# Kernel tuning notes

Measured on AMD Instinct MI355X. Metric: run time of the kernel, lower is better.

The kernel has to match this reference:

```python
import jax, jax.numpy as jnp
import numpy as np

B, T, D, H = 2, 2048, 1024, 16
Hd = D // H


def setup_inputs() -> dict:
    key = jax.random.key(0)
    ks = jax.random.split(key, 9)
    s = 1.0 / np.sqrt(D)
    return {
        "x": jax.random.normal(ks[0], (B, T, D), jnp.float32),
        "Wq": jax.random.normal(ks[1], (D, D), jnp.float32) * s,
        "bq": jax.random.normal(ks[2], (D,), jnp.float32) * 0.01,
        "Wk": jax.random.normal(ks[3], (D, D), jnp.float32) * s,
        "bk": jax.random.normal(ks[4], (D,), jnp.float32) * 0.01,
        "Wv": jax.random.normal(ks[5], (D, D), jnp.float32) * s,
        "bv": jax.random.normal(ks[6], (D,), jnp.float32) * 0.01,
        "Wo": jax.random.normal(ks[7], (D, D), jnp.float32) * s,
        "bo": jax.random.normal(ks[8], (D,), jnp.float32) * 0.01,
    }


def reference(x, Wq, bq, Wk, bk, Wv, bv, Wo, bo):
    # torch Linear: y = x @ W.T + b
    def proj(W, b):
        y = jnp.einsum('btd,ed->bte', x, W) + b          # [B,T,D]
        return y.reshape(B, T, H, Hd).transpose(0, 2, 1, 3)  # [B,H,T,Hd]
    q = proj(Wq, bq) / jnp.sqrt(jnp.asarray(Hd, x.dtype))
    k = proj(Wk, bk)
    v = proj(Wv, bv)
    scores = jnp.einsum('bhqd,bhkd->bhqk', q, k)         # [B,H,T,T]
    attn = jax.nn.softmax(scores, axis=-1)
    out = jnp.einsum('bhqk,bhkd->bhqd', attn, v)         # [B,H,T,Hd]
    out = out.transpose(0, 2, 1, 3).reshape(B, T, D)
    return jnp.einsum('btd,ed->bte', out, Wo) + bo
```

## Files before the change

kernel.cpp:

```cpp
#include <hip/hip_runtime.h>
#include <cmath>

typedef __attribute__((ext_vector_type(8))) short bf16x8;
typedef __attribute__((ext_vector_type(4))) float f32x4;

#define MFMA_BF16 __builtin_amdgcn_mfma_f32_16x16x32_bf16

__device__ __forceinline__ unsigned short f2b(float f) {
  union { float f; unsigned u; } v; v.f = f;
  unsigned r = (v.u + 0x7FFFu + ((v.u >> 16) & 1u)) >> 16;
  return (unsigned short)r;
}

__device__ __forceinline__ unsigned cvt_pk_bf16(float lo, float hi) {
  unsigned r;
  asm("v_cvt_pk_bf16_f32 %0, %1, %2" : "=v"(r) : "v"(lo), "v"(hi));
  return r;
}

__device__ __forceinline__ float fast_exp2(float x) {
  float r;
  asm("v_exp_f32 %0, %1" : "=v"(r) : "v"(x));
  return r;
}

__device__ __forceinline__ void gload_lds16(const void* g, void* l) {
  __builtin_amdgcn_global_load_lds(
      (const __attribute__((address_space(1))) void*)g,
      (__attribute__((address_space(3))) void*)l, 16, 0, 0);
}

__global__ __launch_bounds__(256) void cvt_all(
    const float* __restrict__ x, const float* __restrict__ Wq,
    const float* __restrict__ Wk, const float* __restrict__ Wv,
    const float* __restrict__ Wo,
    unsigned short* __restrict__ xb, unsigned short* __restrict__ wqb,
    unsigned short* __restrict__ wkb, unsigned short* __restrict__ wvb,
    unsigned short* __restrict__ wob) {
  int i = blockIdx.x * 256 + threadIdx.x;
  const float* src; unsigned short* dst; int off;
  if (i < 1048576)      { src = x;  dst = xb;  off = i; }
  else if (i < 1310720) { src = Wq; dst = wqb; off = i - 1048576; }
  else if (i < 1572864) { src = Wk; dst = wkb; off = i - 1310720; }
  else if (i < 1835008) { src = Wv; dst = wvb; off = i - 1572864; }
  else                  { src = Wo; dst = wob; off = i - 1835008; }
  float4 v = reinterpret_cast<const float4*>(src)[off];
  ushort4 o;
  o.x = f2b(v.x); o.y = f2b(v.y); o.z = f2b(v.z); o.w = f2b(v.w);
  reinterpret_cast<ushort4*>(dst)[off] = o;
}

__global__ __launch_bounds__(512, 4) void qkv_gemm(
    const unsigned short* __restrict__ X,
    const unsigned short* __restrict__ Wq, const unsigned short* __restrict__ Wk,
    const unsigned short* __restrict__ Wv,
    const float* __restrict__ bq, const float* __restrict__ bk,
    const float* __restrict__ bv,
    unsigned short* __restrict__ Qo, unsigned short* __restrict__ Ko,
    unsigned short* __restrict__ Vto) {
  __shared__ char smA[2][16384];
  __shared__ char smB[2][16384];
  const int tid = threadIdx.x, lane = tid & 63, wvid = tid >> 6;
  const int g = lane >> 4, l15 = lane & 15;
  const int wr = wvid >> 1, wc = wvid & 1;
  const int lin = blockIdx.y * 32 + blockIdx.x;
  const int xcd = lin & 7, j = lin >> 3;
  const int m_tile = (xcd >> 1) * 8 + (j & 7);
  const int bnall = (xcd & 1) * 12 + (j >> 3);
  const int m0 = m_tile * 128;
  const int wsel = bnall >> 3;
  const int n0 = (bnall & 7) * 128;
  const unsigned short* W = (wsel == 0) ? Wq : (wsel == 1) ? Wk : Wv;
  const float* bias = (wsel == 0) ? bq : (wsel == 1) ? bk : bv;

  f32x4 acc[2][4];
#pragma unroll
  for (int i = 0; i < 2; ++i)
#pragma unroll
    for (int j2 = 0; j2 < 4; ++j2) acc[i][j2] = (f32x4){0.f, 0.f, 0.f, 0.f};

#define QSTAGE(b, kt)                                                          \
  {                                                                            \
    _Pragma("unroll") for (int i = 0; i < 2; ++i) {                            \
      int c = (i * 8 + wvid) * 64 + lane;                                      \
      int row = c >> 3;                                                        \
      int cb = (c & 7) ^ (row & 7);                                            \
      gload_lds16(X + (size_t)(m0 + row) * 1024 + (kt) * 64 + cb * 8,          \
                  smA[b] + (i * 8 + wvid) * 1024);                             \
      gload_lds16(W + (size_t)(n0 + row) * 1024 + (kt) * 64 + cb * 8,          \
                  smB[b] + (i * 8 + wvid) * 1024);                             \
    }                                                                          \
  }

#define QBODY(buf)                                                             \
  {                                                                            \
    bf16x8 af[2][2], bfr[4][2];                                                \
    _Pragma("unroll") for (int mi = 0; mi < 2; ++mi)                           \
      _Pragma("unroll") for (int ks = 0; ks < 2; ++ks) {                       \
        int rowa = wr * 32 + mi * 16 + l15;                                    \
        int addra = (rowa * 128 + ks * 64 + g * 16) ^ ((rowa & 7) << 4);       \
        af[mi][ks] = *(const bf16x8*)(smA[buf] + addra);                       \
      }                                                                        \
    _Pragma("unroll") for (int ni = 0; ni < 4; ++ni)                           \
      _Pragma("unroll") for (int ks = 0; ks < 2; ++ks) {                       \
        int rowb = wc * 64 + ni * 16 + l15;                                    \
        int addrb = (rowb * 128 + ks * 64 + g * 16) ^ ((rowb & 7) << 4);       \
        bfr[ni][ks] = *(const bf16x8*)(smB[buf] + addrb);                      \
      }                                                                        \
    __builtin_amdgcn_s_setprio(1);                                             \
    _Pragma("unroll") for (int ks = 0; ks < 2; ++ks)                           \
      _Pragma("unroll") for (int mi = 0; mi < 2; ++mi)                         \
        _Pragma("unroll") for (int ni = 0; ni < 4; ++ni)                       \
          acc[mi][ni] = MFMA_BF16(af[mi][ks], bfr[ni][ks], acc[mi][ni], 0, 0, 0); \
    __builtin_amdgcn_s_setprio(0);                                             \
  }

  QSTAGE(0, 0);
  QSTAGE(1, 1);
  for (int kt = 0; kt < 15; ++kt) {
    asm volatile("s_waitcnt vmcnt(4)" ::: "memory");
    __builtin_amdgcn_s_barrier();
    __builtin_amdgcn_sched_barrier(0);
    const int buf = kt & 1;
    QBODY(buf);
    __builtin_amdgcn_sched_barrier(0);
    __builtin_amdgcn_s_barrier();
    if (kt < 14) QSTAGE(buf, kt + 2);
  }
  asm volatile("s_waitcnt vmcnt(0)" ::: "memory");
  __builtin_amdgcn_s_barrier();
  __builtin_amdgcn_sched_barrier(0);
  QBODY(1);

  const float qscale = (wsel == 0) ? 0.125f * 1.44269504f : 1.0f;
#pragma unroll
  for (int mi = 0; mi < 2; ++mi)
#pragma unroll
    for (int ni = 0; ni < 4; ++ni)
#pragma unroll
      for (int r = 0; r < 4; ++r) {
        int m = m0 + wr * 32 + mi * 16 + g * 4 + r;
        int n = n0 + wc * 64 + ni * 16 + l15;
        float v = (acc[mi][ni][r] + bias[n]) * qscale;
        int b = m >> 11, t = m & 2047;
        int h = n >> 6, hd = n & 63;
        unsigned short bv16 = f2b(v);
        if (wsel == 2)
          Vto[(((size_t)b * 16 + h) * 64 + hd) * 2048 + t] = bv16;
        else if (wsel == 1)
          Ko[(((size_t)b * 16 + h) * 2048 + t) * 64 + hd] = bv16;
        else
          Qo[(((size_t)b * 16 + h) * 2048 + t) * 64 + hd] = bv16;
      }
}

__global__ __launch_bounds__(512, 4) void attn_kernel(
    const unsigned short* __restrict__ Qg, const unsigned short* __restrict__ Kg,
    const unsigned short* __restrict__ Vtg, unsigned short* __restrict__ Og) {
  __shared__ char smK[2][16384];
  __shared__ char smV[2][16384];
  __shared__ char smPT[8][2048];
  const int tid = threadIdx.x, lane = tid & 63, wvid = tid >> 6;
  const int g = lane >> 4, l15 = lane & 15;
  const int lin = blockIdx.y * 16 + blockIdx.x;
  const int wg = (lin & 7) * 64 + (lin >> 3);
  const int bx = wg & 15, bh = wg >> 4;
  const int q0 = bx * 128 + wvid * 16;
  const unsigned short* Qh = Qg + (size_t)bh * 2048 * 64;
  const unsigned short* Kh = Kg + (size_t)bh * 2048 * 64;
  const unsigned short* Vh = Vtg + (size_t)bh * 64 * 2048;

  bf16x8 qf[2];
#pragma unroll
  for (int ks = 0; ks < 2; ++ks)
    qf[ks] = *(const bf16x8*)(Qh + (size_t)(q0 + l15) * 64 + ks * 32 + g * 8);

  bf16x8 ones;
#pragma unroll
  for (int j = 0; j < 8; ++j) ones[j] = (short)0x3F80;

  f32x4 acc[4];
  f32x4 accL;
#pragma unroll
  for (int di = 0; di < 4; ++di) acc[di] = (f32x4){0.f, 0.f, 0.f, 0.f};
  accL = (f32x4){0.f, 0.f, 0.f, 0.f};

#define STAGE(buf, kt2)                                                        \
  {                                                                            \
    int c = wvid * 64 + lane;                                      \
    int row = c >> 3;                                                          \
    int cbK = (c & 7) ^ (((((row) >> 3) & 3) << 1) | (((row) >> 1) & 1));      \
    int cbV = (c & 7) ^ (row & 7);                                             \
    _Pragma("unroll") for (int s = 0; s < 2; ++s) {                            \
      gload_lds16(Kh + (size_t)((kt2) * 128 + s * 64 + row) * 64 + cbK * 8,    \
                  smK[buf] + s * 8192 + wvid * 1024);                          \
      gload_lds16(Vh + (size_t)row * 2048 + (kt2) * 128 + s * 64 + cbV * 8,    \
                  smV[buf] + s * 8192 + wvid * 1024);                          \
    }                                                                          \
  }

  STAGE(0, 0);
  __syncthreads();
  int buf = 0;
  char* P = smPT[wvid];

  for (int kt2 = 0; kt2 < 16; ++kt2) {
    if (kt2 < 15) STAGE(buf ^ 1, kt2 + 1);

#pragma unroll
    for (int s = 0; s < 2; ++s) {
      const char* Kt = smK[buf] + s * 8192;
      const char* Vt = smV[buf] + s * 8192;

      f32x4 st[4];
#pragma unroll
      for (int ki = 0; ki < 4; ++ki) st[ki] = (f32x4){0.f, 0.f, 0.f, 0.f};
      __builtin_amdgcn_s_setprio(1);
#pragma unroll
      for (int ks = 0; ks < 2; ++ks)
#pragma unroll
        for (int ki = 0; ki < 4; ++ki) {
          int row = ((ki >> 1) << 5) | ((l15 >> 2) << 3) | ((ki & 1) << 2) | (l15 & 3);
          int fk = (((row >> 3) & 3) << 1) | ((row >> 1) & 1);
          int addr = (row * 128 + ks * 64 + g * 16) ^ (fk << 4);
          bf16x8 kb = *(const bf16x8*)(Kt + addr);
          st[ki] = MFMA_BF16(kb, qf[ks], st[ki], 0, 0, 0);
        }
      __builtin_amdgcn_s_setprio(0);

#pragma unroll
      for (int ki = 0; ki < 4; ++ki)
#pragma unroll
        for (int r = 0; r < 4; ++r) st[ki][r] = fast_exp2(st[ki][r]);

#pragma unroll
      for (int ks = 0; ks < 2; ++ks) {
        union { uint4 u; bf16x8 b; } pc;
        pc.u.x = cvt_pk_bf16(st[2 * ks][0], st[2 * ks][1]);
        pc.u.y = cvt_pk_bf16(st[2 * ks][2], st[2 * ks][3]);
        pc.u.z = cvt_pk_bf16(st[2 * ks + 1][0], st[2 * ks + 1][1]);
        pc.u.w = cvt_pk_bf16(st[2 * ks + 1][2], st[2 * ks + 1][3]);
        bf16x8 pb = pc.b;
        __builtin_amdgcn_s_setprio(1);
        accL = MFMA_BF16(ones, pb, accL, 0, 0, 0);
#pragma unroll
        for (int di = 0; di < 4; ++di) {
          int d = di * 16 + l15;
          int vaddr = (d * 128 + ks * 64 + g * 16) ^ ((d & 7) << 4);
          bf16x8 vb = *(const bf16x8*)(Vt + vaddr);
          acc[di] = MFMA_BF16(vb, pb, acc[di], 0, 0, 0);
        }
        __builtin_amdgcn_s_setprio(0);
      }
    }

    __syncthreads();
    buf ^= 1;
  }

  float inv = 1.0f / accL[0];
#pragma unroll
  for (int di = 0; di < 4; ++di) {
    uint2 w;
    w.x = cvt_pk_bf16(acc[di][0] * inv, acc[di][1] * inv);
    w.y = cvt_pk_bf16(acc[di][2] * inv, acc[di][3] * inv);
    int addr = (l15 * 128 + di * 32 + g * 8) ^ ((l15 & 7) << 4);
    *(uint2*)(P + addr) = w;
  }
  __syncthreads();
  const int b = bh >> 4, h = bh & 15;
#pragma unroll
  for (int i = 0; i < 2; ++i) {
    int c = i * 64 + lane;
    int q = c >> 3, cb = c & 7;
    int addr = (q * 128 + cb * 16) ^ ((q & 7) << 4);
    uint4 v = *(const uint4*)(P + addr);
    int t = q0 + q;
    *(uint4*)(Og + ((size_t)(b * 2048 + t)) * 1024 + h * 64 + cb * 8) = v;
  }
}

__global__ __launch_bounds__(512, 4) void out_gemm(
    const unsigned short* __restrict__ A, const unsigned short* __restrict__ W,
    const float* __restrict__ bias, float* __restrict__ out) {
  __shared__ char smA[2][16384];
  __shared__ char smB[2][16384];
  const int tid = threadIdx.x, lane = tid & 63, wvid = tid >> 6;
  const int g = lane >> 4, l15 = lane & 15;
  const int wr = wvid >> 1, wc = wvid & 1;
  const int lin = blockIdx.y * 32 + blockIdx.x;
  const int xcd = lin & 7, j = lin >> 3;
  const int m0 = (xcd * 4 + (j & 3)) * 128;
  const int n0 = (j >> 2) * 128;

  f32x4 acc[2][4];
#pragma unroll
  for (int i = 0; i < 2; ++i)
#pragma unroll
    for (int j2 = 0; j2 < 4; ++j2) acc[i][j2] = (f32x4){0.f, 0.f, 0.f, 0.f};

#define OSTAGE(b, kt)                                                          \
  {                                                                            \
    _Pragma("unroll") for (int i = 0; i < 2; ++i) {                            \
      int c = (i * 8 + wvid) * 64 + lane;                                      \
      int row = c >> 3;                                                        \
      int cb = (c & 7) ^ (row & 7);                                            \
      gload_lds16(A + (size_t)(m0 + row) * 1024 + (kt) * 64 + cb * 8,          \
                  smA[b] + (i * 8 + wvid) * 1024);                             \
      gload_lds16(W + (size_t)(n0 + row) * 1024 + (kt) * 64 + cb * 8,          \
                  smB[b] + (i * 8 + wvid) * 1024);                             \
    }                                                                          \
  }

#define OBODY(buf)                                                             \
  {                                                                            \
    bf16x8 af[2][2], bfr[4][2];                                                \
    _Pragma("unroll") for (int mi = 0; mi < 2; ++mi)                           \
      _Pragma("unroll") for (int ks = 0; ks < 2; ++ks) {                       \
        int rowa = wr * 32 + mi * 16 + l15;                                    \
        int addra = (rowa * 128 + ks * 64 + g * 16) ^ ((rowa & 7) << 4);       \
        af[mi][ks] = *(const bf16x8*)(smA[buf] + addra);                       \
      }                                                                        \
    _Pragma("unroll") for (int ni = 0; ni < 4; ++ni)                           \
      _Pragma("unroll") for (int ks = 0; ks < 2; ++ks) {                       \
        int rowb = wc * 64 + ni * 16 + l15;                                    \
        int addrb = (rowb * 128 + ks * 64 + g * 16) ^ ((rowb & 7) << 4);       \
        bfr[ni][ks] = *(const bf16x8*)(smB[buf] + addrb);                      \
      }                                                                        \
    __builtin_amdgcn_s_setprio(1);                                             \
    _Pragma("unroll") for (int ks = 0; ks < 2; ++ks)                           \
      _Pragma("unroll") for (int mi = 0; mi < 2; ++mi)                         \
        _Pragma("unroll") for (int ni = 0; ni < 4; ++ni)                       \
          acc[mi][ni] = MFMA_BF16(af[mi][ks], bfr[ni][ks], acc[mi][ni], 0, 0, 0); \
    __builtin_amdgcn_s_setprio(0);                                             \
  }

  OSTAGE(0, 0);
  OSTAGE(1, 1);
  for (int kt = 0; kt < 15; ++kt) {
    asm volatile("s_waitcnt vmcnt(4)" ::: "memory");
    __builtin_amdgcn_s_barrier();
    __builtin_amdgcn_sched_barrier(0);
    const int buf = kt & 1;
    OBODY(buf);
    __builtin_amdgcn_sched_barrier(0);
    __builtin_amdgcn_s_barrier();
    if (kt < 14) OSTAGE(buf, kt + 2);
  }
  asm volatile("s_waitcnt vmcnt(0)" ::: "memory");
  __builtin_amdgcn_s_barrier();
  __builtin_amdgcn_sched_barrier(0);
  OBODY(1);

#pragma unroll
  for (int mi = 0; mi < 2; ++mi)
#pragma unroll
    for (int ni = 0; ni < 4; ++ni)
#pragma unroll
      for (int r = 0; r < 4; ++r) {
        int mm = m0 + wr * 32 + mi * 16 + g * 4 + r;
        int nn = n0 + wc * 64 + ni * 16 + l15;
        out[(size_t)mm * 1024 + nn] = acc[mi][ni][r] + bias[nn];
      }
}

extern "C" void kernel_launch(void* const* d_in, const int* in_sizes, int n_in,
                              void* d_out, int out_size, void* d_ws, size_t ws_size,
                              hipStream_t stream) {
  const float* x = (const float*)d_in[0];
  const float* Wq = (const float*)d_in[1];
  const float* bq = (const float*)d_in[2];
  const float* Wk = (const float*)d_in[3];
  const float* bk = (const float*)d_in[4];
  const float* Wv = (const float*)d_in[5];
  const float* bv = (const float*)d_in[6];
  const float* Wo = (const float*)d_in[7];
  const float* bo = (const float*)d_in[8];
  float* out = (float*)d_out;
  char* ws = (char*)d_ws;

  unsigned short* xb = (unsigned short*)(ws + 0);
  unsigned short* Ob = (unsigned short*)(ws + 0);
  unsigned short* wqb = (unsigned short*)(ws + 8388608);
  unsigned short* wkb = (unsigned short*)(ws + 10485760);
  unsigned short* wvb = (unsigned short*)(ws + 12582912);
  unsigned short* wob = (unsigned short*)(ws + 14680064);
  unsigned short* Qb = (unsigned short*)(ws + 16777216);
  unsigned short* Kb = (unsigned short*)(ws + 25165824);
  unsigned short* Vtb = (unsigned short*)(ws + 33554432);

  hipLaunchKernelGGL(cvt_all, dim3(8192), dim3(256), 0, stream,
                     x, Wq, Wk, Wv, Wo, xb, wqb, wkb, wvb, wob);
  hipLaunchKernelGGL(qkv_gemm, dim3(32, 24), dim3(512), 0, stream, xb, wqb, wkb, wvb,
                     bq, bk, bv, Qb, Kb, Vtb);
  hipLaunchKernelGGL(attn_kernel, dim3(16, 32), dim3(512), 0, stream, Qb, Kb, Vtb, Ob);
  hipLaunchKernelGGL(out_gemm, dim3(32, 8), dim3(512), 0, stream, Ob, wob, bo, out);
}
```

Before: 107.0 us.

## Enlarge QKV GEMM tiles to 256x256 with dynamic LDS double buffering

The QKV projection GEMM moves from 128x128 tiles (768 blocks) to 256x256 tiles (192 blocks). Each wave now computes a 128x64 sub-tile with 32 accumulators, using 128KB of dynamic shared memory split into two ping-pong buffers. The aim is higher arithmetic intensity and less global/LDS traffic per FLOP. In exchange, occupancy drops (launch bounds 2, fewer blocks than CUs may leave some CUs idle), register pressure rises, and the pipeline now waits with vmcnt(0) each half-step.

```diff
diff --git a/kernel.cpp b/kernel.cpp
--- a/kernel.cpp
+++ b/kernel.cpp
@@ -50,7 +50,9 @@
   reinterpret_cast<ushort4*>(dst)[off] = o;
 }
 
-__global__ __launch_bounds__(512, 4) void qkv_gemm(
+#define LOFF(b, mat, h) ((((b)*2 + (mat))*2 + (h)) * 16384)
+
+__global__ __launch_bounds__(512, 2) void qkv_gemm(
     const unsigned short* __restrict__ X,
     const unsigned short* __restrict__ Wq, const unsigned short* __restrict__ Wk,
     const unsigned short* __restrict__ Wv,
@@ -58,90 +60,101 @@
     const float* __restrict__ bv,
     unsigned short* __restrict__ Qo, unsigned short* __restrict__ Ko,
     unsigned short* __restrict__ Vto) {
-  __shared__ char smA[2][16384];
-  __shared__ char smB[2][16384];
+  extern __shared__ char sm[];
   const int tid = threadIdx.x, lane = tid & 63, wvid = tid >> 6;
   const int g = lane >> 4, l15 = lane & 15;
-  const int wr = wvid >> 1, wc = wvid & 1;
-  const int lin = blockIdx.y * 32 + blockIdx.x;
+  const int wr = wvid >> 2;
+  const int wc = wvid & 3;
+  const int hb = wc >> 1;
+  const int lrB0 = (wc & 1) * 64;
+  const int lin = blockIdx.x;
   const int xcd = lin & 7, j = lin >> 3;
-  const int m_tile = (xcd >> 1) * 8 + (j & 7);
-  const int bnall = (xcd & 1) * 12 + (j >> 3);
-  const int m0 = m_tile * 128;
-  const int wsel = bnall >> 3;
-  const int n0 = (bnall & 7) * 128;
+  const int m_tile = (xcd >> 1) * 4 + (j & 3);
+  const int nt = (xcd & 1) * 6 + (j >> 2);
+  const int m0 = m_tile * 256;
+  const int wsel = nt >> 2;
+  const int n0 = (nt & 3) * 256;
   const unsigned short* W = (wsel == 0) ? Wq : (wsel == 1) ? Wk : Wv;
   const float* bias = (wsel == 0) ? bq : (wsel == 1) ? bk : bv;
 
-  f32x4 acc[2][4];
-#pragma unroll
-  for (int i = 0; i < 2; ++i)
-#pragma unroll
-    for (int j2 = 0; j2 < 4; ++j2) acc[i][j2] = (f32x4){0.f, 0.f, 0.f, 0.f};
-
-#define QSTAGE(b, kt)                                                          \
+  const unsigned short* Arow = X + (size_t)m0 * 1024;
+  const unsigned short* Brow = W + (size_t)n0 * 1024;
+
+  f32x4 acc[8][4];
+#pragma unroll
+  for (int a = 0; a < 8; ++a)
+#pragma unroll
+    for (int b = 0; b < 4; ++b) acc[a][b] = (f32x4){0.f, 0.f, 0.f, 0.f};
+
+#define ST(b, mat, h, kt)                                                      \
   {                                                                            \
-    _Pragma("unroll") for (int i = 0; i < 2; ++i) {                            \
-      int c = (i * 8 + wvid) * 64 + lane;                                      \
-      int row = c >> 3;                                                        \
-      int cb = (c & 7) ^ (row & 7);                                            \
-      gload_lds16(X + (size_t)(m0 + row) * 1024 + (kt) * 64 + cb * 8,          \
-                  smA[b] + (i * 8 + wvid) * 1024);                             \
-      gload_lds16(W + (size_t)(n0 + row) * 1024 + (kt) * 64 + cb * 8,          \
-                  smB[b] + (i * 8 + wvid) * 1024);                             \
+    const unsigned short* base =                                               \
+        (mat) ? (Brow + (size_t)(h) * 128 * 1024)                              \
+              : (Arow + (size_t)(h) * 128 * 1024);                             \
+    _Pragma("unroll") for (int ii = 0; ii < 2; ++ii) {                         \
+      int c = ii * 512 + tid;                                                  \
+      int lr = c >> 3;                                                         \
+      int cb = (c & 7) ^ (lr & 7);                                             \
+      gload_lds16(base + (size_t)lr * 1024 + (kt) * 64 + cb * 8,               \
+                  sm + LOFF(b, mat, h) + ii * 8192 + wvid * 1024);             \
     }                                                                          \
   }
 
-#define QBODY(buf)                                                             \
+#define QCOMP(bufi)                                                            \
   {                                                                            \
-    bf16x8 af[2][2], bfr[4][2];                                                \
-    _Pragma("unroll") for (int mi = 0; mi < 2; ++mi)                           \
-      _Pragma("unroll") for (int ks = 0; ks < 2; ++ks) {                       \
-        int rowa = wr * 32 + mi * 16 + l15;                                    \
-        int addra = (rowa * 128 + ks * 64 + g * 16) ^ ((rowa & 7) << 4);       \
-        af[mi][ks] = *(const bf16x8*)(smA[buf] + addra);                       \
+    const char* Ab = sm + LOFF(bufi, 0, wr);                                   \
+    const char* Bb = sm + LOFF(bufi, 1, hb);                                   \
+    _Pragma("unroll") for (int ph = 0; ph < 4; ++ph) {                         \
+      const int mh = ph >> 1, ks = ph & 1;                                     \
+      bf16x8 af[4], bfr[4];                                                    \
+      _Pragma("unroll") for (int mi = 0; mi < 4; ++mi) {                       \
+        int lr = mh * 64 + mi * 16 + l15;                                      \
+        af[mi] = *(const bf16x8*)(Ab +                                         \
+                 ((lr * 128 + ks * 64 + g * 16) ^ ((lr & 7) << 4)));           \
       }                                                                        \
-    _Pragma("unroll") for (int ni = 0; ni < 4; ++ni)                           \
-      _Pragma("unroll") for (int ks = 0; ks < 2; ++ks) {                       \
-        int rowb = wc * 64 + ni * 16 + l15;                                    \
-        int addrb = (rowb * 128 + ks * 64 + g * 16) ^ ((rowb & 7) << 4);       \
-        bfr[ni][ks] = *(const bf16x8*)(smB[buf] + addrb);                      \
+      _Pragma("unroll") for (int ni = 0; ni < 4; ++ni) {                       \
+        int lr = lrB0 + ni * 16 + l15;                                         \
+        bfr[ni] = *(const bf16x8*)(Bb +                                        \
+                  ((lr * 128 + ks * 64 + g * 16) ^ ((lr & 7) << 4)));          \
       }                                                                        \
-    __builtin_amdgcn_s_setprio(1);                                             \
-    _Pragma("unroll") for (int ks = 0; ks < 2; ++ks)                           \
-      _Pragma("unroll") for (int mi = 0; mi < 2; ++mi)                         \
-        _Pragma("unroll") for (int ni = 0; ni < 4; ++ni)                       \
-          acc[mi][ni] = MFMA_BF16(af[mi][ks], bfr[ni][ks], acc[mi][ni], 0, 0, 0); \
-    __builtin_amdgcn_s_setprio(0);                                             \
-  }
-
-  QSTAGE(0, 0);
-  QSTAGE(1, 1);
-  for (int kt = 0; kt < 15; ++kt) {
-    asm volatile("s_waitcnt vmcnt(4)" ::: "memory");
+      __builtin_amdgcn_s_setprio(1);                                           \
+      _Pragma("unroll") for (int ni = 0; ni < 4; ++ni)                         \
+        _Pragma("unroll") for (int mi = 0; mi < 4; ++mi)                       \
+          acc[mh * 4 + mi][ni] =                                               \
+              MFMA_BF16(af[mi], bfr[ni], acc[mh * 4 + mi][ni], 0, 0, 0);       \
+      __builtin_amdgcn_s_setprio(0);                                           \
+    }                                                                          \
+  }
+
+  ST(0, 0, 0, 0); ST(0, 0, 1, 0); ST(0, 1, 0, 0); ST(0, 1, 1, 0);
+
+  for (int i = 0; i < 8; ++i) {
+    asm volatile("s_waitcnt vmcnt(0)" ::: "memory");
     __builtin_amdgcn_s_barrier();
     __builtin_amdgcn_sched_barrier(0);
-    const int buf = kt & 1;
-    QBODY(buf);
+    ST(1, 0, 0, 2 * i + 1); ST(1, 0, 1, 2 * i + 1);
+    ST(1, 1, 0, 2 * i + 1); ST(1, 1, 1, 2 * i + 1);
+    QCOMP(0);
+    asm volatile("s_waitcnt vmcnt(0)" ::: "memory");
+    __builtin_amdgcn_s_barrier();
     __builtin_amdgcn_sched_barrier(0);
-    __builtin_amdgcn_s_barrier();
-    if (kt < 14) QSTAGE(buf, kt + 2);
-  }
-  asm volatile("s_waitcnt vmcnt(0)" ::: "memory");
-  __builtin_amdgcn_s_barrier();
-  __builtin_amdgcn_sched_barrier(0);
-  QBODY(1);
+    if (i < 7) {
+      ST(0, 0, 0, 2 * i + 2); ST(0, 0, 1, 2 * i + 2);
+      ST(0, 1, 0, 2 * i + 2); ST(0, 1, 1, 2 * i + 2);
+    }
+    QCOMP(1);
+  }
 
   const float qscale = (wsel == 0) ? 0.125f * 1.44269504f : 1.0f;
 #pragma unroll
-  for (int mi = 0; mi < 2; ++mi)
+  for (int mi8 = 0; mi8 < 8; ++mi8)
 #pragma unroll
     for (int ni = 0; ni < 4; ++ni)
 #pragma unroll
       for (int r = 0; r < 4; ++r) {
-        int m = m0 + wr * 32 + mi * 16 + g * 4 + r;
+        int m = m0 + wr * 128 + mi8 * 16 + g * 4 + r;
         int n = n0 + wc * 64 + ni * 16 + l15;
-        float v = (acc[mi][ni][r] + bias[n]) * qscale;
+        float v = (acc[mi8][ni][r] + bias[n]) * qscale;
         int b = m >> 11, t = m & 2047;
         int h = n >> 6, hd = n & 63;
         unsigned short bv16 = f2b(v);
@@ -389,9 +402,12 @@
   unsigned short* Kb = (unsigned short*)(ws + 25165824);
   unsigned short* Vtb = (unsigned short*)(ws + 33554432);
 
+  hipFuncSetAttribute((const void*)qkv_gemm,
+                      hipFuncAttributeMaxDynamicSharedMemorySize, 131072);
+
   hipLaunchKernelGGL(cvt_all, dim3(8192), dim3(256), 0, stream,
                      x, Wq, Wk, Wv, Wo, xb, wqb, wkb, wvb, wob);
-  hipLaunchKernelGGL(qkv_gemm, dim3(32, 24), dim3(512), 0, stream, xb, wqb, wkb, wvb,
+  hipLaunchKernelGGL(qkv_gemm, dim3(192), dim3(512), 131072, stream, xb, wqb, wkb, wvb,
                      bq, bk, bv, Qb, Kb, Vtb);
   hipLaunchKernelGGL(attn_kernel, dim3(16, 32), dim3(512), 0, stream, Qb, Kb, Vtb, Ob);
   hipLaunchKernelGGL(out_gemm, dim3(32, 8), dim3(512), 0, stream, Ob, wob, bo, out);
```

After: 123.1 us. 15.0% more time.

## Prefetch two K/V tiles ahead with explicit vmcnt waits in attention loop

Applied to the files above, without the earlier changes.

Restructures the attention K/V loop so two tiles are in flight at once. Each iteration now waits only for the older tile's async loads (vmcnt(4)) instead of draining all loads at __syncthreads, and it reloads the buffer just consumed with tile kt2+2. This is meant to hide global-to-LDS latency behind the MFMA and exp work. It relies on hand-set waitcnt counts and sched_barriers, which is fragile if the compiler emits other vector memory ops.

```diff
diff --git a/kernel.cpp b/kernel.cpp
--- a/kernel.cpp
+++ b/kernel.cpp
@@ -199,64 +199,66 @@
     }                                                                          \
   }
 
+#define ABODY(buf)                                                             \
+  {                                                                            \
+    _Pragma("unroll") for (int s = 0; s < 2; ++s) {                            \
+      const char* Kt = smK[buf] + s * 8192;                                    \
+      const char* Vt = smV[buf] + s * 8192;                                    \
+      f32x4 st[4];                                                             \
+      _Pragma("unroll") for (int ki = 0; ki < 4; ++ki)                         \
+        st[ki] = (f32x4){0.f, 0.f, 0.f, 0.f};                                  \
+      __builtin_amdgcn_s_setprio(1);                                           \
+      _Pragma("unroll") for (int ks = 0; ks < 2; ++ks)                         \
+        _Pragma("unroll") for (int ki = 0; ki < 4; ++ki) {                     \
+          int row = ((ki >> 1) << 5) | ((l15 >> 2) << 3) | ((ki & 1) << 2) |   \
+                    (l15 & 3);                                                 \
+          int fk = (((row >> 3) & 3) << 1) | ((row >> 1) & 1);                 \
+          int addr = (row * 128 + ks * 64 + g * 16) ^ (fk << 4);               \
+          bf16x8 kb = *(const bf16x8*)(Kt + addr);                             \
+          st[ki] = MFMA_BF16(kb, qf[ks], st[ki], 0, 0, 0);                     \
+        }                                                                      \
+      __builtin_amdgcn_s_setprio(0);                                           \
+      _Pragma("unroll") for (int ki = 0; ki < 4; ++ki)                         \
+        _Pragma("unroll") for (int r = 0; r < 4; ++r)                          \
+          st[ki][r] = fast_exp2(st[ki][r]);                                    \
+      _Pragma("unroll") for (int ks = 0; ks < 2; ++ks) {                       \
+        union { uint4 u; bf16x8 b; } pc;                                       \
+        pc.u.x = cvt_pk_bf16(st[2 * ks][0], st[2 * ks][1]);                    \
+        pc.u.y = cvt_pk_bf16(st[2 * ks][2], st[2 * ks][3]);                    \
+        pc.u.z = cvt_pk_bf16(st[2 * ks + 1][0], st[2 * ks + 1][1]);            \
+        pc.u.w = cvt_pk_bf16(st[2 * ks + 1][2], st[2 * ks + 1][3]);            \
+        bf16x8 pb = pc.b;                                                      \
+        __builtin_amdgcn_s_setprio(1);                                         \
+        accL = MFMA_BF16(ones, pb, accL, 0, 0, 0);                             \
+        _Pragma("unroll") for (int di = 0; di < 4; ++di) {                     \
+          int d = di * 16 + l15;                                               \
+          int vaddr = (d * 128 + ks * 64 + g * 16) ^ ((d & 7) << 4);           \
+          bf16x8 vb = *(const bf16x8*)(Vt + vaddr);                            \
+          acc[di] = MFMA_BF16(vb, pb, acc[di], 0, 0, 0);                       \
+        }                                                                      \
+        __builtin_amdgcn_s_setprio(0);                                         \
+      }                                                                        \
+    }                                                                          \
+  }
+
   STAGE(0, 0);
-  __syncthreads();
-  int buf = 0;
+  STAGE(1, 1);
   char* P = smPT[wvid];
 
-  for (int kt2 = 0; kt2 < 16; ++kt2) {
-    if (kt2 < 15) STAGE(buf ^ 1, kt2 + 1);
-
-#pragma unroll
-    for (int s = 0; s < 2; ++s) {
-      const char* Kt = smK[buf] + s * 8192;
-      const char* Vt = smV[buf] + s * 8192;
-
-      f32x4 st[4];
-#pragma unroll
-      for (int ki = 0; ki < 4; ++ki) st[ki] = (f32x4){0.f, 0.f, 0.f, 0.f};
-      __builtin_amdgcn_s_setprio(1);
-#pragma unroll
-      for (int ks = 0; ks < 2; ++ks)
-#pragma unroll
-        for (int ki = 0; ki < 4; ++ki) {
-          int row = ((ki >> 1) << 5) | ((l15 >> 2) << 3) | ((ki & 1) << 2) | (l15 & 3);
-          int fk = (((row >> 3) & 3) << 1) | ((row >> 1) & 1);
-          int addr = (row * 128 + ks * 64 + g * 16) ^ (fk << 4);
-          bf16x8 kb = *(const bf16x8*)(Kt + addr);
-          st[ki] = MFMA_BF16(kb, qf[ks], st[ki], 0, 0, 0);
-        }
-      __builtin_amdgcn_s_setprio(0);
-
-#pragma unroll
-      for (int ki = 0; ki < 4; ++ki)
-#pragma unroll
-        for (int r = 0; r < 4; ++r) st[ki][r] = fast_exp2(st[ki][r]);
-
-#pragma unroll
-      for (int ks = 0; ks < 2; ++ks) {
-        union { uint4 u; bf16x8 b; } pc;
-        pc.u.x = cvt_pk_bf16(st[2 * ks][0], st[2 * ks][1]);
-        pc.u.y = cvt_pk_bf16(st[2 * ks][2], st[2 * ks][3]);
-        pc.u.z = cvt_pk_bf16(st[2 * ks + 1][0], st[2 * ks + 1][1]);
-        pc.u.w = cvt_pk_bf16(st[2 * ks + 1][2], st[2 * ks + 1][3]);
-        bf16x8 pb = pc.b;
-        __builtin_amdgcn_s_setprio(1);
-        accL = MFMA_BF16(ones, pb, accL, 0, 0, 0);
-#pragma unroll
-        for (int di = 0; di < 4; ++di) {
-          int d = di * 16 + l15;
-          int vaddr = (d * 128 + ks * 64 + g * 16) ^ ((d & 7) << 4);
-          bf16x8 vb = *(const bf16x8*)(Vt + vaddr);
-          acc[di] = MFMA_BF16(vb, pb, acc[di], 0, 0, 0);
-        }
-        __builtin_amdgcn_s_setprio(0);
-      }
-    }
-
-    __syncthreads();
-    buf ^= 1;
-  }
+  for (int kt2 = 0; kt2 < 15; ++kt2) {
+    asm volatile("s_waitcnt vmcnt(4)" ::: "memory");
+    __builtin_amdgcn_s_barrier();
+    __builtin_amdgcn_sched_barrier(0);
+    const int buf = kt2 & 1;
+    ABODY(buf);
+    __builtin_amdgcn_sched_barrier(0);
+    __builtin_amdgcn_s_barrier();
+    if (kt2 < 14) STAGE(buf, kt2 + 2);
+  }
+  asm volatile("s_waitcnt vmcnt(0)" ::: "memory");
+  __builtin_amdgcn_s_barrier();
+  __builtin_amdgcn_sched_barrier(0);
+  ABODY(1);
 
   float inv = 1.0f / accL[0];
 #pragma unroll
```

After: 108.5 us. About the same (+1.4%).

## Retile QKV GEMM to 128x192 tiles spanning fused Q/K/V weight columns

Applied to the files above, without the earlier changes.

The QKV projection GEMM moves from 128x128 output tiles (768 blocks) to 128x192 tiles over a concatenated N=3072 dimension (512 blocks). A tile can now straddle Wq/Wk/Wv, so the weight pointer, bias and scale are chosen per row and per column. The wave layout changes from 4x2 to 2x4, with each wave computing 64x48. The aim is more reuse of the staged X tile and one full wave of blocks, at the cost of more LDS and accumulator registers per block and per-element selection logic in the epilogue.

```diff
diff --git a/kernel.cpp b/kernel.cpp
--- a/kernel.cpp
+++ b/kernel.cpp
@@ -59,58 +59,63 @@
     unsigned short* __restrict__ Qo, unsigned short* __restrict__ Ko,
     unsigned short* __restrict__ Vto) {
   __shared__ char smA[2][16384];
-  __shared__ char smB[2][16384];
+  __shared__ char smB[2][24576];
   const int tid = threadIdx.x, lane = tid & 63, wvid = tid >> 6;
   const int g = lane >> 4, l15 = lane & 15;
-  const int wr = wvid >> 1, wc = wvid & 1;
-  const int lin = blockIdx.y * 32 + blockIdx.x;
+  const int wr = wvid >> 2;
+  const int wc = wvid & 3;
+  const int lin = blockIdx.x;
   const int xcd = lin & 7, j = lin >> 3;
   const int m_tile = (xcd >> 1) * 8 + (j & 7);
-  const int bnall = (xcd & 1) * 12 + (j >> 3);
+  const int pt = (xcd & 1) * 8 + (j >> 3);
   const int m0 = m_tile * 128;
-  const int wsel = bnall >> 3;
-  const int n0 = (bnall & 7) * 128;
-  const unsigned short* W = (wsel == 0) ? Wq : (wsel == 1) ? Wk : Wv;
-  const float* bias = (wsel == 0) ? bq : (wsel == 1) ? bk : bv;
-
-  f32x4 acc[2][4];
-#pragma unroll
-  for (int i = 0; i < 2; ++i)
-#pragma unroll
-    for (int j2 = 0; j2 < 4; ++j2) acc[i][j2] = (f32x4){0.f, 0.f, 0.f, 0.f};
+  const int pn0 = pt * 192;
+
+  f32x4 acc[4][3];
+#pragma unroll
+  for (int i = 0; i < 4; ++i)
+#pragma unroll
+    for (int j2 = 0; j2 < 3; ++j2) acc[i][j2] = (f32x4){0.f, 0.f, 0.f, 0.f};
 
 #define QSTAGE(b, kt)                                                          \
   {                                                                            \
     _Pragma("unroll") for (int i = 0; i < 2; ++i) {                            \
-      int c = (i * 8 + wvid) * 64 + lane;                                      \
+      int c = i * 512 + tid;                                                   \
       int row = c >> 3;                                                        \
       int cb = (c & 7) ^ (row & 7);                                            \
       gload_lds16(X + (size_t)(m0 + row) * 1024 + (kt) * 64 + cb * 8,          \
-                  smA[b] + (i * 8 + wvid) * 1024);                             \
-      gload_lds16(W + (size_t)(n0 + row) * 1024 + (kt) * 64 + cb * 8,          \
-                  smB[b] + (i * 8 + wvid) * 1024);                             \
+                  smA[b] + i * 8192 + wvid * 1024);                            \
+    }                                                                          \
+    _Pragma("unroll") for (int i = 0; i < 3; ++i) {                            \
+      int c = i * 512 + tid;                                                   \
+      int row = c >> 3;                                                        \
+      int cb = (c & 7) ^ (row & 7);                                            \
+      int n = pn0 + row;                                                       \
+      const unsigned short* wp = (n < 1024) ? Wq : (n < 2048) ? Wk : Wv;       \
+      gload_lds16(wp + (size_t)(n & 1023) * 1024 + (kt) * 64 + cb * 8,         \
+                  smB[b] + i * 8192 + wvid * 1024);                            \
     }                                                                          \
   }
 
 #define QBODY(buf)                                                             \
   {                                                                            \
-    bf16x8 af[2][2], bfr[4][2];                                                \
-    _Pragma("unroll") for (int mi = 0; mi < 2; ++mi)                           \
+    bf16x8 af[4][2], bfr[3][2];                                                \
+    _Pragma("unroll") for (int mi = 0; mi < 4; ++mi)                           \
       _Pragma("unroll") for (int ks = 0; ks < 2; ++ks) {                       \
-        int rowa = wr * 32 + mi * 16 + l15;                                    \
+        int rowa = wr * 64 + mi * 16 + l15;                                    \
         int addra = (rowa * 128 + ks * 64 + g * 16) ^ ((rowa & 7) << 4);       \
         af[mi][ks] = *(const bf16x8*)(smA[buf] + addra);                       \
       }                                                                        \
-    _Pragma("unroll") for (int ni = 0; ni < 4; ++ni)                           \
+    _Pragma("unroll") for (int ni = 0; ni < 3; ++ni)                           \
       _Pragma("unroll") for (int ks = 0; ks < 2; ++ks) {                       \
-        int rowb = wc * 64 + ni * 16 + l15;                                    \
+        int rowb = wc * 48 + ni * 16 + l15;                                    \
         int addrb = (rowb * 128 + ks * 64 + g * 16) ^ ((rowb & 7) << 4);       \
         bfr[ni][ks] = *(const bf16x8*)(smB[buf] + addrb);                      \
       }                                                                        \
     __builtin_amdgcn_s_setprio(1);                                             \
     _Pragma("unroll") for (int ks = 0; ks < 2; ++ks)                           \
-      _Pragma("unroll") for (int mi = 0; mi < 2; ++mi)                         \
-        _Pragma("unroll") for (int ni = 0; ni < 4; ++ni)                       \
+      _Pragma("unroll") for (int mi = 0; mi < 4; ++mi)                         \
+        _Pragma("unroll") for (int ni = 0; ni < 3; ++ni)                       \
           acc[mi][ni] = MFMA_BF16(af[mi][ks], bfr[ni][ks], acc[mi][ni], 0, 0, 0); \
     __builtin_amdgcn_s_setprio(0);                                             \
   }
@@ -118,7 +123,7 @@
   QSTAGE(0, 0);
   QSTAGE(1, 1);
   for (int kt = 0; kt < 15; ++kt) {
-    asm volatile("s_waitcnt vmcnt(4)" ::: "memory");
+    asm volatile("s_waitcnt vmcnt(5)" ::: "memory");
     __builtin_amdgcn_s_barrier();
     __builtin_amdgcn_sched_barrier(0);
     const int buf = kt & 1;
@@ -132,18 +137,20 @@
   __builtin_amdgcn_sched_barrier(0);
   QBODY(1);
 
-  const float qscale = (wsel == 0) ? 0.125f * 1.44269504f : 1.0f;
-#pragma unroll
-  for (int mi = 0; mi < 2; ++mi)
-#pragma unroll
-    for (int ni = 0; ni < 4; ++ni)
+#pragma unroll
+  for (int mi = 0; mi < 4; ++mi)
+#pragma unroll
+    for (int ni = 0; ni < 3; ++ni)
 #pragma unroll
       for (int r = 0; r < 4; ++r) {
-        int m = m0 + wr * 32 + mi * 16 + g * 4 + r;
-        int n = n0 + wc * 64 + ni * 16 + l15;
-        float v = (acc[mi][ni][r] + bias[n]) * qscale;
+        int m = m0 + wr * 64 + mi * 16 + g * 4 + r;
+        int n = pn0 + wc * 48 + ni * 16 + l15;
+        int wsel = n >> 10, nl = n & 1023;
+        float bias = (wsel == 0) ? bq[nl] : (wsel == 1) ? bk[nl] : bv[nl];
+        float qscale = (wsel == 0) ? 0.125f * 1.44269504f : 1.0f;
+        float v = (acc[mi][ni][r] + bias) * qscale;
         int b = m >> 11, t = m & 2047;
-        int h = n >> 6, hd = n & 63;
+        int h = nl >> 6, hd = nl & 63;
         unsigned short bv16 = f2b(v);
         if (wsel == 2)
           Vto[(((size_t)b * 16 + h) * 64 + hd) * 2048 + t] = bv16;
@@ -391,7 +398,7 @@
 
   hipLaunchKernelGGL(cvt_all, dim3(8192), dim3(256), 0, stream,
                      x, Wq, Wk, Wv, Wo, xb, wqb, wkb, wvb, wob);
-  hipLaunchKernelGGL(qkv_gemm, dim3(32, 24), dim3(512), 0, stream, xb, wqb, wkb, wvb,
+  hipLaunchKernelGGL(qkv_gemm, dim3(512), dim3(512), 0, stream, xb, wqb, wkb, wvb,
                      bq, bk, bv, Qb, Kb, Vtb);
   hipLaunchKernelGGL(attn_kernel, dim3(16, 32), dim3(512), 0, stream, Qb, Kb, Vtb, Ob);
   hipLaunchKernelGGL(out_gemm, dim3(32, 8), dim3(512), 0, stream, Ob, wob, bo, out);
```

Measured after the change: 129.8 us (median of 2 runs). 21.3% more time.
